# Kernel optimization log

Measured on AMD Instinct MI355X. Metric: run time of the kernel, lower is better.

The kernel has to match this reference:

```python
import jax, jax.numpy as jnp
import numpy as np

B, H, S, DK = 4, 16, 2048, 128

def setup_inputs() -> dict:
    key = jax.random.key(0)
    kq, kk, kv, km = jax.random.split(key, 4)
    query = jax.random.normal(kq, (B, H, S, DK), dtype=jnp.float32)
    key_t = jax.random.normal(kk, (B, H, S, DK), dtype=jnp.float32)
    value = jax.random.normal(kv, (B, H, S, DK), dtype=jnp.float32)
    mask = jax.random.randint(km, (B, H, S, S), 0, 2, dtype=jnp.int32)
    return {"query": query, "key": key_t, "value": value, "mask": mask}

def reference(query, key, value, mask):
    d_k = query.shape[-1]
    # scores: (b, h, sq, sk)
    scores = jnp.einsum("bhqd,bhkd->bhqk", query, key) / jnp.sqrt(jnp.float32(d_k))
    scores = jnp.where(mask == 0, -jnp.inf, scores)
    weights = jax.nn.softmax(scores, axis=-1)  # dropout p=0.0 -> identity
    out = jnp.einsum("bhqk,bhkd->bhqd", weights, value)
    return out, weights
```

## Files before the change

### kernel.cpp

```cpp
#include <hip/hip_runtime.h>


constexpr int Sc = 2048, Dc = 128;
constexpr int BHc = 64;
constexpr long OUTE = (long)BHc * Sc * Dc;
constexpr long KVE  = (long)BHc * Sc * Dc;
constexpr int QBR = 128;
constexpr int NQT = Sc / QBR;
constexpr int NBLK = BHc * NQT;
#define SCALEF 0.088388347648318447f

typedef __attribute__((ext_vector_type(4))) float f32x4;
typedef _Float16 f16x8 __attribute__((ext_vector_type(8)));

static __device__ __forceinline__ f16x8 loadcvt8h(const float* __restrict__ p) {
  float4 a = *(const float4*)p;
  float4 b = *(const float4*)(p + 4);
  f16x8 r;
  r[0] = (_Float16)a.x; r[1] = (_Float16)a.y; r[2] = (_Float16)a.z; r[3] = (_Float16)a.w;
  r[4] = (_Float16)b.x; r[5] = (_Float16)b.y; r[6] = (_Float16)b.z; r[7] = (_Float16)b.w;
  return r;
}

__global__ __launch_bounds__(256)
void kconv_kernel(const float* __restrict__ K, _Float16* __restrict__ Kh) {
  long i = ((long)blockIdx.x * 256 + threadIdx.x) * 8;
  f16x8 v = loadcvt8h(K + i);
  *(f16x8*)(Kh + i) = v;
}

__global__ __launch_bounds__(256)
void vtrans_kernel(const float* __restrict__ V, _Float16* __restrict__ Vt) {
  __shared__ _Float16 sT[Dc][64 + 2];
  const int bh = blockIdx.x >> 5;
  const int kt = blockIdx.x & 31;
  const int tid = threadIdx.x;
  const float* vb = V + ((long)bh * Sc + kt * 64) * Dc;
  #pragma unroll
  for (int i = 0; i < 8; i++) {
    int e = tid + i * 256;
    int ki = e >> 5;
    int dq = (e & 31) * 4;
    float4 f = *(const float4*)(vb + (long)ki * Dc + dq);
    sT[dq + 0][ki] = (_Float16)f.x;
    sT[dq + 1][ki] = (_Float16)f.y;
    sT[dq + 2][ki] = (_Float16)f.z;
    sT[dq + 3][ki] = (_Float16)f.w;
  }
  __syncthreads();
  #pragma unroll
  for (int i = 0; i < 4; i++) {
    int chunk = tid + i * 256;
    int d = chunk >> 3;
    int kc = (chunk & 7) * 8;
    f16x8 o;
    #pragma unroll
    for (int j = 0; j < 8; j++) o[j] = sT[d][kc + j];
    *(f16x8*)(Vt + ((long)bh * Dc + d) * Sc + kt * 64 + kc) = o;
  }
}

__global__ __launch_bounds__(512, 4)
void sdpa_main(const float* __restrict__ Qg, const int* __restrict__ Mg,
               float* __restrict__ Og, const _Float16* __restrict__ Kh,
               const _Float16* __restrict__ Vt) {
  __shared__ __align__(16) _Float16 sK[64][136];
  __shared__ __align__(16) _Float16 sV[128][72];
  __shared__ __align__(16) _Float16 sPw[8][16][72];
  __shared__ float sRinv[QBR];

  const int bid0 = blockIdx.x;
  const int bid  = (bid0 & 7) * (NBLK >> 3) + (bid0 >> 3);
  const int bh = bid >> 4;
  const int qt = bid & (NQT - 1);

  const int tid  = threadIdx.x;
  const int lane = tid & 63;
  const int w = tid >> 6;
  const int g = lane >> 4;
  const int c = lane & 15;

  f16x8 aq[4];
  {
    const float* qp = Qg + ((long)bh * Sc + (long)qt * QBR + w * 16 + c) * Dc + g * 8;
    #pragma unroll
    for (int ch = 0; ch < 4; ch++) aq[ch] = loadcvt8h(qp + ch * 32);
  }

  const _Float16* Kplane = Kh + (long)bh * Sc * Dc;
  const _Float16* Vplane = Vt + (long)bh * Dc * Sc;
  const int* Mwave = Mg + ((long)bh * Sc + (long)qt * QBR + w * 16 + g * 4) * Sc;

  const int kr0 = tid >> 4, kd0 = tid & 15;
  const int vr0 = tid >> 3, vc0 = tid & 7;

  auto loadK = [&](int cc, f16x8& a, f16x8& b) {
    a = *(const f16x8*)(Kplane + (long)(cc * 64 + kr0) * Dc + kd0 * 8);
    b = *(const f16x8*)(Kplane + (long)(cc * 64 + kr0 + 32) * Dc + kd0 * 8);
  };
  auto stageK = [&](const f16x8& a, const f16x8& b) {
    *(f16x8*)&sK[kr0][kd0 * 8] = a;
    *(f16x8*)&sK[kr0 + 32][kd0 * 8] = b;
  };
  auto loadV = [&](int cc, f16x8& a, f16x8& b) {
    a = *(const f16x8*)(Vplane + (long)vr0 * Sc + cc * 64 + vc0 * 8);
    b = *(const f16x8*)(Vplane + (long)(vr0 + 64) * Sc + cc * 64 + vc0 * 8);
  };
  auto stageV = [&](const f16x8& a, const f16x8& b) {
    *(f16x8*)&sV[vr0][vc0 * 8] = a;
    *(f16x8*)&sV[vr0 + 64][vc0 * 8] = b;
  };

  auto qkTile = [&](int nt) -> f32x4 {
    const _Float16* kb = &sK[nt * 16 + c][g * 8];
    f16x8 b0 = *(const f16x8*)kb;
    f16x8 b1 = *(const f16x8*)(kb + 32);
    f16x8 b2 = *(const f16x8*)(kb + 64);
    f16x8 b3 = *(const f16x8*)(kb + 96);
    f32x4 s = {0.f, 0.f, 0.f, 0.f};
    s = __builtin_amdgcn_mfma_f32_16x16x32_f16(aq[0], b0, s, 0, 0, 0);
    s = __builtin_amdgcn_mfma_f32_16x16x32_f16(aq[1], b1, s, 0, 0, 0);
    s = __builtin_amdgcn_mfma_f32_16x16x32_f16(aq[2], b2, s, 0, 0, 0);
    s = __builtin_amdgcn_mfma_f32_16x16x32_f16(aq[3], b3, s, 0, 0, 0);
    return s;
  };

  float rs[4] = {0.f, 0.f, 0.f, 0.f};
  {
    f16x8 ka, kb2;
    loadK(0, ka, kb2);
    for (int cc = 0; cc < 32; cc++) {
      __syncthreads();
      stageK(ka, kb2);
      __syncthreads();
      if (cc + 1 < 32) loadK(cc + 1, ka, kb2);
      int mv[4][4];
      const int* mp = Mwave + cc * 64 + c;
      #pragma unroll
      for (int nt = 0; nt < 4; nt++)
        #pragma unroll
        for (int r = 0; r < 4; r++)
          mv[nt][r] = mp[(long)r * Sc + nt * 16];
      #pragma unroll
      for (int nt = 0; nt < 4; nt++) {
        f32x4 s = qkTile(nt);
        #pragma unroll
        for (int r = 0; r < 4; r++) {
          float e = (mv[nt][r] != 0) ? __expf(s[r] * SCALEF) : 0.f;
          rs[r] += (float)(_Float16)e;
        }
      }
    }
  }
  #pragma unroll
  for (int r = 0; r < 4; r++) {
    float x = rs[r];
    x += __shfl_xor(x, 1);
    x += __shfl_xor(x, 2);
    x += __shfl_xor(x, 4);
    x += __shfl_xor(x, 8);
    if (c == 0) sRinv[w * 16 + g * 4 + r] = (x > 0.f) ? (1.f / x) : 0.f;
  }
  __syncthreads();
  const float rinvW = sRinv[w * 16 + (lane >> 2)];
  float rinvO[4];
  #pragma unroll
  for (int r = 0; r < 4; r++) rinvO[r] = sRinv[w * 16 + g * 4 + r];

  f32x4 oacc[8];
  #pragma unroll
  for (int dt = 0; dt < 8; dt++) oacc[dt] = (f32x4){0.f, 0.f, 0.f, 0.f};
  float* wbase = Og + OUTE + ((long)bh * Sc + (long)qt * QBR + w * 16) * Sc;
  const int wr = lane >> 2;
  const int wq = lane & 3;

  {
    f16x8 ka, kb2, va, vb2;
    loadK(0, ka, kb2);
    loadV(0, va, vb2);
    for (int cc = 0; cc < 32; cc++) {
      __syncthreads();
      stageK(ka, kb2);
      stageV(va, vb2);
      __syncthreads();
      if (cc + 1 < 32) {
        loadK(cc + 1, ka, kb2);
        loadV(cc + 1, va, vb2);
      }
      int mv[4][4];
      const int* mp = Mwave + cc * 64 + c;
      #pragma unroll
      for (int nt = 0; nt < 4; nt++)
        #pragma unroll
        for (int r = 0; r < 4; r++)
          mv[nt][r] = mp[(long)r * Sc + nt * 16];
      #pragma unroll
      for (int nt = 0; nt < 4; nt++) {
        f32x4 s = qkTile(nt);
        #pragma unroll
        for (int r = 0; r < 4; r++) {
          float e = (mv[nt][r] != 0) ? __expf(s[r] * SCALEF) : 0.f;
          sPw[w][g * 4 + r][nt * 16 + c] = (_Float16)e;
        }
      }
      {
        f16x8 p0 = *(const f16x8*)&sPw[w][wr][wq * 16];
        f16x8 p1 = *(const f16x8*)&sPw[w][wr][wq * 16 + 8];
        float* dst = wbase + (long)wr * Sc + cc * 64 + wq * 16;
        float4 o0, o1, o2, o3;
        o0.x = (float)p0[0] * rinvW; o0.y = (float)p0[1] * rinvW;
        o0.z = (float)p0[2] * rinvW; o0.w = (float)p0[3] * rinvW;
        o1.x = (float)p0[4] * rinvW; o1.y = (float)p0[5] * rinvW;
        o1.z = (float)p0[6] * rinvW; o1.w = (float)p0[7] * rinvW;
        o2.x = (float)p1[0] * rinvW; o2.y = (float)p1[1] * rinvW;
        o2.z = (float)p1[2] * rinvW; o2.w = (float)p1[3] * rinvW;
        o3.x = (float)p1[4] * rinvW; o3.y = (float)p1[5] * rinvW;
        o3.z = (float)p1[6] * rinvW; o3.w = (float)p1[7] * rinvW;
        *(float4*)dst = o0;
        *(float4*)(dst + 4) = o1;
        *(float4*)(dst + 8) = o2;
        *(float4*)(dst + 12) = o3;
      }
      f16x8 pa0 = *(const f16x8*)&sPw[w][c][g * 8];
      f16x8 pa1 = *(const f16x8*)&sPw[w][c][32 + g * 8];
      #pragma unroll
      for (int dt = 0; dt < 8; dt++) {
        const _Float16* vb = &sV[dt * 16 + c][g * 8];
        f16x8 v0 = *(const f16x8*)vb;
        f16x8 v1 = *(const f16x8*)(vb + 32);
        oacc[dt] = __builtin_amdgcn_mfma_f32_16x16x32_f16(pa0, v0, oacc[dt], 0, 0, 0);
        oacc[dt] = __builtin_amdgcn_mfma_f32_16x16x32_f16(pa1, v1, oacc[dt], 0, 0, 0);
      }
    }
  }

  float* ob = Og + ((long)bh * Sc + (long)qt * QBR + w * 16 + g * 4) * Dc;
  #pragma unroll
  for (int r = 0; r < 4; r++) {
    #pragma unroll
    for (int dt = 0; dt < 8; dt++) {
      ob[(long)r * Dc + dt * 16 + c] = oacc[dt][r] * rinvO[r];
    }
  }
}

__global__ __launch_bounds__(256)
void sdpa_naive(const float* __restrict__ Qg, const float* __restrict__ Kg,
                const float* __restrict__ Vg, const int* __restrict__ Mg,
                float* __restrict__ Og) {
  __shared__ float sE[4][Sc];
  const int bh = blockIdx.x >> 9;
  const int rg = blockIdx.x & 511;
  const int wv = threadIdx.x >> 6, ln = threadIdx.x & 63;
  const int qrow = rg * 4 + wv;
  const float* qp = Qg + ((long)bh * Sc + qrow) * Dc;
  const int* mp = Mg + ((long)bh * Sc + qrow) * Sc;
  float rsum = 0.f;
  for (int k0 = 0; k0 < Sc; k0 += 64) {
    const int kcol = k0 + ln;
    const float* kp = Kg + ((long)bh * Sc + kcol) * Dc;
    float s = 0.f;
    for (int d = 0; d < Dc; d++) s += qp[d] * kp[d];
    float e = (mp[kcol] != 0) ? __expf(s * SCALEF) : 0.f;
    e = (float)(_Float16)e;
    sE[wv][kcol] = e;
    rsum += e;
  }
  for (int o = 1; o < 64; o <<= 1) rsum += __shfl_xor(rsum, o);
  float oa = 0.f, ob2 = 0.f;
  for (int k = 0; k < Sc; k++) {
    const float e = sE[wv][k];
    const float* vp = Vg + ((long)bh * Sc + k) * Dc;
    oa += e * vp[ln];
    ob2 += e * vp[ln + 64];
  }
  const float ri = (rsum > 0.f) ? 1.f / rsum : 0.f;
  float* op = Og + ((long)bh * Sc + qrow) * Dc;
  op[ln] = oa * ri;
  op[ln + 64] = ob2 * ri;
  float* wb = Og + OUTE + ((long)bh * Sc + qrow) * Sc;
  for (int k = ln; k < Sc; k += 64) wb[k] = sE[wv][k] * ri;
}

extern "C" void kernel_launch(void* const* d_in, const int* in_sizes, int n_in,
                              void* d_out, int out_size, void* d_ws, size_t ws_size,
                              hipStream_t stream) {
  (void)in_sizes; (void)n_in; (void)out_size;
  const float* q = (const float*)d_in[0];
  const float* k = (const float*)d_in[1];
  const float* v = (const float*)d_in[2];
  const int* m = (const int*)d_in[3];
  float* out = (float*)d_out;

  const size_t need = 2UL * KVE * sizeof(_Float16);
  if (d_ws != nullptr && ws_size >= need) {
    _Float16* Kh = (_Float16*)d_ws;
    _Float16* Vt = Kh + KVE;
    hipLaunchKernelGGL(kconv_kernel, dim3((int)(KVE / 8 / 256)), dim3(256), 0, stream, k, Kh);
    hipLaunchKernelGGL(vtrans_kernel, dim3(BHc * 32), dim3(256), 0, stream, v, Vt);
    hipLaunchKernelGGL(sdpa_main, dim3(NBLK), dim3(512), 0, stream, q, m, out, Kh, Vt);
  } else {
    hipLaunchKernelGGL(sdpa_naive, dim3(BHc * 512), dim3(256), 0, stream, q, k, v, m, out);
  }
}
```

Baseline: 794.9 us.

## Cache mask as register bitmask across passes and raise MFMA wave priority

The first pass packs each chunk's 16 mask values into bits of a 16-entry register array, so the second pass reads the mask from registers instead of reloading int32 mask data from global memory. The chunk loops are split into two unrolled halves of 16 so the bitmask array can be indexed statically. s_setprio is also raised around the MFMA sequences to favour matrix-issuing waves. The unrolling and extra live registers may raise register pressure and cut occupancy.

```diff
diff --git a/kernel.cpp b/kernel.cpp
--- a/kernel.cpp
+++ b/kernel.cpp
@@ -118,36 +118,52 @@
     f16x8 b2 = *(const f16x8*)(kb + 64);
     f16x8 b3 = *(const f16x8*)(kb + 96);
     f32x4 s = {0.f, 0.f, 0.f, 0.f};
+    __builtin_amdgcn_s_setprio(1);
     s = __builtin_amdgcn_mfma_f32_16x16x32_f16(aq[0], b0, s, 0, 0, 0);
     s = __builtin_amdgcn_mfma_f32_16x16x32_f16(aq[1], b1, s, 0, 0, 0);
     s = __builtin_amdgcn_mfma_f32_16x16x32_f16(aq[2], b2, s, 0, 0, 0);
     s = __builtin_amdgcn_mfma_f32_16x16x32_f16(aq[3], b3, s, 0, 0, 0);
+    __builtin_amdgcn_s_setprio(0);
     return s;
   };
 
   float rs[4] = {0.f, 0.f, 0.f, 0.f};
+  unsigned ms[16];
   {
     f16x8 ka, kb2;
     loadK(0, ka, kb2);
-    for (int cc = 0; cc < 32; cc++) {
-      __syncthreads();
-      stageK(ka, kb2);
-      __syncthreads();
-      if (cc + 1 < 32) loadK(cc + 1, ka, kb2);
-      int mv[4][4];
-      const int* mp = Mwave + cc * 64 + c;
+    for (int cp = 0; cp < 2; cp++) {
+      const int shbase = cp * 16;
       #pragma unroll
-      for (int nt = 0; nt < 4; nt++)
-        #pragma unroll
-        for (int r = 0; r < 4; r++)
-          mv[nt][r] = mp[(long)r * Sc + nt * 16];
-      #pragma unroll
-      for (int nt = 0; nt < 4; nt++) {
-        f32x4 s = qkTile(nt);
-        #pragma unroll
-        for (int r = 0; r < 4; r++) {
-          float e = (mv[nt][r] != 0) ? __expf(s[r] * SCALEF) : 0.f;
-          rs[r] += (float)(_Float16)e;
+      for (int ci = 0; ci < 16; ci++) {
+        const int cc = cp * 16 + ci;
+        __syncthreads();
+        stageK(ka, kb2);
+        __syncthreads();
+        if (cc + 1 < 32) loadK(cc + 1, ka, kb2);
+        int mv[4][4];
+        const int* mp = Mwave + cc * 64 + c;
+        #pragma unroll
+        for (int nt = 0; nt < 4; nt++)
+          #pragma unroll
+          for (int r = 0; r < 4; r++)
+            mv[nt][r] = mp[(long)r * Sc + nt * 16];
+        unsigned bits = 0;
+        #pragma unroll
+        for (int nt = 0; nt < 4; nt++)
+          #pragma unroll
+          for (int r = 0; r < 4; r++)
+            bits |= (mv[nt][r] != 0 ? 1u : 0u) << (nt * 4 + r);
+        if (cp == 0) ms[ci] = bits;
+        else ms[ci] |= bits << shbase;
+        #pragma unroll
+        for (int nt = 0; nt < 4; nt++) {
+          f32x4 s = qkTile(nt);
+          #pragma unroll
+          for (int r = 0; r < 4; r++) {
+            float e = ((bits >> (nt * 4 + r)) & 1u) ? __expf(s[r] * SCALEF) : 0.f;
+            rs[r] += (float)(_Float16)e;
+          }
         }
       }
     }
@@ -178,58 +194,59 @@
     f16x8 ka, kb2, va, vb2;
     loadK(0, ka, kb2);
     loadV(0, va, vb2);
-    for (int cc = 0; cc < 32; cc++) {
-      __syncthreads();
-      stageK(ka, kb2);
-      stageV(va, vb2);
-      __syncthreads();
-      if (cc + 1 < 32) {
-        loadK(cc + 1, ka, kb2);
-        loadV(cc + 1, va, vb2);
-      }
-      int mv[4][4];
-      const int* mp = Mwave + cc * 64 + c;
+    for (int cp = 0; cp < 2; cp++) {
+      const int shbase = cp * 16;
       #pragma unroll
-      for (int nt = 0; nt < 4; nt++)
-        #pragma unroll
-        for (int r = 0; r < 4; r++)
-          mv[nt][r] = mp[(long)r * Sc + nt * 16];
-      #pragma unroll
-      for (int nt = 0; nt < 4; nt++) {
-        f32x4 s = qkTile(nt);
-        #pragma unroll
-        for (int r = 0; r < 4; r++) {
-          float e = (mv[nt][r] != 0) ? __expf(s[r] * SCALEF) : 0.f;
-          sPw[w][g * 4 + r][nt * 16 + c] = (_Float16)e;
-        }
-      }
-      {
-        f16x8 p0 = *(const f16x8*)&sPw[w][wr][wq * 16];
-        f16x8 p1 = *(const f16x8*)&sPw[w][wr][wq * 16 + 8];
-        float* dst = wbase + (long)wr * Sc + cc * 64 + wq * 16;
-        float4 o0, o1, o2, o3;
-        o0.x = (float)p0[0] * rinvW; o0.y = (float)p0[1] * rinvW;
-        o0.z = (float)p0[2] * rinvW; o0.w = (float)p0[3] * rinvW;
-        o1.x = (float)p0[4] * rinvW; o1.y = (float)p0[5] * rinvW;
-        o1.z = (float)p0[6] * rinvW; o1.w = (float)p0[7] * rinvW;
-        o2.x = (float)p1[0] * rinvW; o2.y = (float)p1[1] * rinvW;
-        o2.z = (float)p1[2] * rinvW; o2.w = (float)p1[3] * rinvW;
-        o3.x = (float)p1[4] * rinvW; o3.y = (float)p1[5] * rinvW;
-        o3.z = (float)p1[6] * rinvW; o3.w = (float)p1[7] * rinvW;
-        *(float4*)dst = o0;
-        *(float4*)(dst + 4) = o1;
-        *(float4*)(dst + 8) = o2;
-        *(float4*)(dst + 12) = o3;
-      }
-      f16x8 pa0 = *(const f16x8*)&sPw[w][c][g * 8];
-      f16x8 pa1 = *(const f16x8*)&sPw[w][c][32 + g * 8];
-      #pragma unroll
-      for (int dt = 0; dt < 8; dt++) {
-        const _Float16* vb = &sV[dt * 16 + c][g * 8];
-        f16x8 v0 = *(const f16x8*)vb;
-        f16x8 v1 = *(const f16x8*)(vb + 32);
-        oacc[dt] = __builtin_amdgcn_mfma_f32_16x16x32_f16(pa0, v0, oacc[dt], 0, 0, 0);
-        oacc[dt] = __builtin_amdgcn_mfma_f32_16x16x32_f16(pa1, v1, oacc[dt], 0, 0, 0);
+      for (int ci = 0; ci < 16; ci++) {
+        const int cc = cp * 16 + ci;
+        __syncthreads();
+        stageK(ka, kb2);
+        stageV(va, vb2);
+        __syncthreads();
+        if (cc + 1 < 32) {
+          loadK(cc + 1, ka, kb2);
+          loadV(cc + 1, va, vb2);
+        }
+        const unsigned bits = ms[ci] >> shbase;
+        #pragma unroll
+        for (int nt = 0; nt < 4; nt++) {
+          f32x4 s = qkTile(nt);
+          #pragma unroll
+          for (int r = 0; r < 4; r++) {
+            float e = ((bits >> (nt * 4 + r)) & 1u) ? __expf(s[r] * SCALEF) : 0.f;
+            sPw[w][g * 4 + r][nt * 16 + c] = (_Float16)e;
+          }
+        }
+        {
+          f16x8 p0 = *(const f16x8*)&sPw[w][wr][wq * 16];
+          f16x8 p1 = *(const f16x8*)&sPw[w][wr][wq * 16 + 8];
+          float* dst = wbase + (long)wr * Sc + cc * 64 + wq * 16;
+          float4 o0, o1, o2, o3;
+          o0.x = (float)p0[0] * rinvW; o0.y = (float)p0[1] * rinvW;
+          o0.z = (float)p0[2] * rinvW; o0.w = (float)p0[3] * rinvW;
+          o1.x = (float)p0[4] * rinvW; o1.y = (float)p0[5] * rinvW;
+          o1.z = (float)p0[6] * rinvW; o1.w = (float)p0[7] * rinvW;
+          o2.x = (float)p1[0] * rinvW; o2.y = (float)p1[1] * rinvW;
+          o2.z = (float)p1[2] * rinvW; o2.w = (float)p1[3] * rinvW;
+          o3.x = (float)p1[4] * rinvW; o3.y = (float)p1[5] * rinvW;
+          o3.z = (float)p1[6] * rinvW; o3.w = (float)p1[7] * rinvW;
+          *(float4*)dst = o0;
+          *(float4*)(dst + 4) = o1;
+          *(float4*)(dst + 8) = o2;
+          *(float4*)(dst + 12) = o3;
+        }
+        f16x8 pa0 = *(const f16x8*)&sPw[w][c][g * 8];
+        f16x8 pa1 = *(const f16x8*)&sPw[w][c][32 + g * 8];
+        __builtin_amdgcn_s_setprio(1);
+        #pragma unroll
+        for (int dt = 0; dt < 8; dt++) {
+          const _Float16* vb = &sV[dt * 16 + c][g * 8];
+          f16x8 v0 = *(const f16x8*)vb;
+          f16x8 v1 = *(const f16x8*)(vb + 32);
+          oacc[dt] = __builtin_amdgcn_mfma_f32_16x16x32_f16(pa0, v0, oacc[dt], 0, 0, 0);
+          oacc[dt] = __builtin_amdgcn_mfma_f32_16x16x32_f16(pa1, v1, oacc[dt], 0, 0, 0);
+        }
+        __builtin_amdgcn_s_setprio(0);
       }
     }
   }
```

New measurement: 2.071 ms. +160.5%, slower.

## Compress mask to bitfield in first pass and double-buffer K smem

Applied to the files above, without the earlier changes.

The first pass (row-sum computation) packs each thread's 16 mask bits per tile into a 32-bit word pair and writes it to a workspace buffer. The second pass reads these packed bits instead of re-reading the int32 mask from global memory, which removes about half of the mask read traffic (the mask is the largest input). The first pass also double-buffers K in shared memory so that one of the two __syncthreads per iteration can be dropped. In exchange, the kernel needs extra workspace and shared memory, which may reduce occupancy.

```diff
diff --git a/kernel.cpp b/kernel.cpp
--- a/kernel.cpp
+++ b/kernel.cpp
@@ -63,8 +63,8 @@
 __global__ __launch_bounds__(512, 4)
 void sdpa_main(const float* __restrict__ Qg, const int* __restrict__ Mg,
                float* __restrict__ Og, const _Float16* __restrict__ Kh,
-               const _Float16* __restrict__ Vt) {
-  __shared__ __align__(16) _Float16 sK[64][136];
+               const _Float16* __restrict__ Vt, unsigned* __restrict__ msk) {
+  __shared__ __align__(16) _Float16 sKd[2][64][136];
   __shared__ __align__(16) _Float16 sV[128][72];
   __shared__ __align__(16) _Float16 sPw[8][16][72];
   __shared__ float sRinv[QBR];
@@ -90,6 +90,7 @@
   const _Float16* Kplane = Kh + (long)bh * Sc * Dc;
   const _Float16* Vplane = Vt + (long)bh * Dc * Sc;
   const int* Mwave = Mg + ((long)bh * Sc + (long)qt * QBR + w * 16 + g * 4) * Sc;
+  unsigned* mskB = msk + (long)bid0 * (16 * 512);
 
   const int kr0 = tid >> 4, kd0 = tid & 15;
   const int vr0 = tid >> 3, vc0 = tid & 7;
@@ -98,9 +99,9 @@
     a = *(const f16x8*)(Kplane + (long)(cc * 64 + kr0) * Dc + kd0 * 8);
     b = *(const f16x8*)(Kplane + (long)(cc * 64 + kr0 + 32) * Dc + kd0 * 8);
   };
-  auto stageK = [&](const f16x8& a, const f16x8& b) {
-    *(f16x8*)&sK[kr0][kd0 * 8] = a;
-    *(f16x8*)&sK[kr0 + 32][kd0 * 8] = b;
+  auto stageK = [&](int p, const f16x8& a, const f16x8& b) {
+    *(f16x8*)&sKd[p][kr0][kd0 * 8] = a;
+    *(f16x8*)&sKd[p][kr0 + 32][kd0 * 8] = b;
   };
   auto loadV = [&](int cc, f16x8& a, f16x8& b) {
     a = *(const f16x8*)(Vplane + (long)vr0 * Sc + cc * 64 + vc0 * 8);
@@ -111,8 +112,8 @@
     *(f16x8*)&sV[vr0 + 64][vc0 * 8] = b;
   };
 
-  auto qkTile = [&](int nt) -> f32x4 {
-    const _Float16* kb = &sK[nt * 16 + c][g * 8];
+  auto qkTile = [&](int p, int nt) -> f32x4 {
+    const _Float16* kb = &sKd[p][nt * 16 + c][g * 8];
     f16x8 b0 = *(const f16x8*)kb;
     f16x8 b1 = *(const f16x8*)(kb + 32);
     f16x8 b2 = *(const f16x8*)(kb + 64);
@@ -129,9 +130,10 @@
   {
     f16x8 ka, kb2;
     loadK(0, ka, kb2);
+    unsigned bpair = 0;
     for (int cc = 0; cc < 32; cc++) {
-      __syncthreads();
-      stageK(ka, kb2);
+      const int p = cc & 1;
+      stageK(p, ka, kb2);
       __syncthreads();
       if (cc + 1 < 32) loadK(cc + 1, ka, kb2);
       int mv[4][4];
@@ -141,12 +143,20 @@
         #pragma unroll
         for (int r = 0; r < 4; r++)
           mv[nt][r] = mp[(long)r * Sc + nt * 16];
+      unsigned bits = 0;
+      #pragma unroll
+      for (int nt = 0; nt < 4; nt++)
+        #pragma unroll
+        for (int r = 0; r < 4; r++)
+          bits |= (mv[nt][r] != 0 ? 1u : 0u) << (nt * 4 + r);
+      if ((cc & 1) == 0) bpair = bits;
+      else mskB[((cc >> 1) << 9) + tid] = bpair | (bits << 16);
       #pragma unroll
       for (int nt = 0; nt < 4; nt++) {
-        f32x4 s = qkTile(nt);
+        f32x4 s = qkTile(p, nt);
         #pragma unroll
         for (int r = 0; r < 4; r++) {
-          float e = (mv[nt][r] != 0) ? __expf(s[r] * SCALEF) : 0.f;
+          float e = ((bits >> (nt * 4 + r)) & 1u) ? __expf(s[r] * SCALEF) : 0.f;
           rs[r] += (float)(_Float16)e;
         }
       }
@@ -178,28 +188,24 @@
     f16x8 ka, kb2, va, vb2;
     loadK(0, ka, kb2);
     loadV(0, va, vb2);
+    unsigned bp = 0;
     for (int cc = 0; cc < 32; cc++) {
       __syncthreads();
-      stageK(ka, kb2);
+      stageK(0, ka, kb2);
       stageV(va, vb2);
       __syncthreads();
       if (cc + 1 < 32) {
         loadK(cc + 1, ka, kb2);
         loadV(cc + 1, va, vb2);
       }
-      int mv[4][4];
-      const int* mp = Mwave + cc * 64 + c;
-      #pragma unroll
-      for (int nt = 0; nt < 4; nt++)
-        #pragma unroll
-        for (int r = 0; r < 4; r++)
-          mv[nt][r] = mp[(long)r * Sc + nt * 16];
+      if ((cc & 1) == 0) bp = mskB[((cc >> 1) << 9) + tid];
+      const unsigned bits = (cc & 1) ? (bp >> 16) : (bp & 0xffffu);
       #pragma unroll
       for (int nt = 0; nt < 4; nt++) {
-        f32x4 s = qkTile(nt);
+        f32x4 s = qkTile(0, nt);
         #pragma unroll
         for (int r = 0; r < 4; r++) {
-          float e = (mv[nt][r] != 0) ? __expf(s[r] * SCALEF) : 0.f;
+          float e = ((bits >> (nt * 4 + r)) & 1u) ? __expf(s[r] * SCALEF) : 0.f;
           sPw[w][g * 4 + r][nt * 16 + c] = (_Float16)e;
         }
       }
@@ -292,13 +298,14 @@
   const int* m = (const int*)d_in[3];
   float* out = (float*)d_out;
 
-  const size_t need = 2UL * KVE * sizeof(_Float16);
+  const size_t need = 2UL * KVE * sizeof(_Float16) + (size_t)NBLK * 16 * 512 * 4;
   if (d_ws != nullptr && ws_size >= need) {
     _Float16* Kh = (_Float16*)d_ws;
     _Float16* Vt = Kh + KVE;
+    unsigned* msk = (unsigned*)(Vt + KVE);
     hipLaunchKernelGGL(kconv_kernel, dim3((int)(KVE / 8 / 256)), dim3(256), 0, stream, k, Kh);
     hipLaunchKernelGGL(vtrans_kernel, dim3(BHc * 32), dim3(256), 0, stream, v, Vt);
-    hipLaunchKernelGGL(sdpa_main, dim3(NBLK), dim3(512), 0, stream, q, m, out, Kh, Vt);
+    hipLaunchKernelGGL(sdpa_main, dim3(NBLK), dim3(512), 0, stream, q, m, out, Kh, Vt, msk);
   } else {
     hipLaunchKernelGGL(sdpa_naive, dim3(BHc * 512), dim3(256), 0, stream, q, k, v, m, out);
   }
```

Result: faster. 704.9 us (-11.3%).
